# Kernel tuning notes

Measured on AMD Instinct MI355X. Metric: run time of the kernel, lower is better.

Reference implementation:

```python
import jax, jax.numpy as jnp
import numpy as np
import math

COV_WEIGHT = 1.0
BANDWIDTH_FACTOR = 1.06
SQRT_2PI = math.sqrt(2.0 * math.pi)
EPS_LOG = 1e-8
H_MIN = 1e-4


def setup_inputs() -> dict:
    key = jax.random.key(0)
    activity = jax.random.normal(key, (2048, 64), dtype=jnp.float32)
    return {"activity": activity}


def reference(activity):
    B, R = activity.shape
    # Silverman bandwidth per receptor (torch .std uses ddof=1)
    std = jnp.std(activity, axis=0, ddof=1)                     # (R,)
    h = jnp.maximum(BANDWIDTH_FACTOR * std * (B ** (-0.2)), H_MIN)  # (R,)

    # Pairwise Gaussian KDE: query == samples == activity
    u = (activity[:, None, :] - activity[None, :, :]) / h       # (B_q, B_s, R)
    kernel_values = jnp.exp(-0.5 * u * u) / SQRT_2PI             # (B_q, B_s, R)
    density = kernel_values.sum(axis=1) / (B * h)                # (B_q, R)

    entropies = -jnp.mean(jnp.log(density + EPS_LOG), axis=0)    # (R,)
    loss_entropy = -entropies.mean()

    # Covariance penalty: sum of squared off-diagonals
    centered = activity - activity.mean(axis=0, keepdims=True)
    cov = (centered.T @ centered) / (B - 1)                      # (R, R)
    off = cov - jnp.diag(jnp.diag(cov))
    loss_cov = jnp.sum(off * off)

    total_loss = loss_entropy + COV_WEIGHT * loss_cov
    return total_loss
```

## Files before the change

### kernel.cpp

```cpp
#include <hip/hip_runtime.h>
#include <math.h>

#define B_SZ 2048
#define R_SZ 64
#define QT 8
#define KDE_BLOCKS (B_SZ / QT)

#define B_POW_NEG02 0.217637640824031f
#define SQRT_2PI 2.5066282746310002f
#define LOG2E 1.44269504088896340736f

extern "C" __device__ float __ocml_native_exp2_f32(float);

typedef __attribute__((ext_vector_type(2))) float f32x2;


__global__ __launch_bounds__(1024) void stats_gram_kernel(const float* __restrict__ A,
                                                          float* __restrict__ qsums,
                                                          float* __restrict__ qsums2,
                                                          float* __restrict__ gram4,
                                                          float* __restrict__ ent_acc,
                                                          int* __restrict__ done_cnt) {
    int b = blockIdx.x;
    int i = b >> 2, qd = b & 3;
    int tid = threadIdx.x;
    int j = tid & 63, bg = tid >> 6;

    const float* __restrict__ Aq = A + (qd * 512) * R_SZ;
    float g = 0.f, sj = 0.f, s2j = 0.f;
#pragma unroll 4
    for (int t = bg; t < 512; t += 16) {
        float ai = Aq[t * R_SZ + i];
        float aj = Aq[t * R_SZ + j];
        g = fmaf(ai, aj, g);
        sj += aj;
        s2j = fmaf(aj, aj, s2j);
    }

    __shared__ float gred[16][64], sred[16][64], s2red[16][64];
    gred[bg][j] = g; sred[bg][j] = sj; s2red[bg][j] = s2j;
    __syncthreads();
    if (tid < 64) {
        float G = 0.f, S = 0.f, S2 = 0.f;
#pragma unroll
        for (int t = 0; t < 16; ++t) { G += gred[t][j]; S += sred[t][j]; S2 += s2red[t][j]; }
        gram4[b * 64 + j] = G;
        if (i == 0) {
            qsums[qd * 64 + j]  = S;
            qsums2[qd * 64 + j] = S2;
        }
    }
    if (b == 0 && tid == 64) { *ent_acc = 0.f; *done_cnt = 0; }
}

__global__ __launch_bounds__(1024) void kde_kernel(const float* __restrict__ A,
                                                   const float* __restrict__ qsums,
                                                   const float* __restrict__ qsums2,
                                                   const float* __restrict__ gram4,
                                                   float* __restrict__ ent_acc,
                                                   int* __restrict__ done_cnt,
                                                   float* __restrict__ out) {
    int tid = threadIdx.x;
    int r = tid & 63, sg = tid >> 6;

    __shared__ float k0s[64], lscs[64], sums_s[64];
    if (tid < 64) {
        float S  = qsums[tid]  + qsums[64 + tid]  + qsums[128 + tid]  + qsums[192 + tid];
        float S2 = qsums2[tid] + qsums2[64 + tid] + qsums2[128 + tid] + qsums2[192 + tid];
        float m = S * (1.f / (float)B_SZ);
        float var = (S2 - S * m) * (1.f / (float)(B_SZ - 1));
        var = fmaxf(var, 0.f);
        float h = fmaxf(1.06f * sqrtf(var) * B_POW_NEG02, 1e-4f);
        k0s[tid]  = sqrtf(0.5f * LOG2E) / h;
        lscs[tid] = 1.0f / ((float)B_SZ * h * SQRT_2PI);
        sums_s[tid] = S;
    }
    __syncthreads();
    float k0 = k0s[r];

    int q0 = blockIdx.x * QT;
    f32x2 uq01 = { A[(q0 + 0) * R_SZ + r] * k0, A[(q0 + 1) * R_SZ + r] * k0 };
    f32x2 uq23 = { A[(q0 + 2) * R_SZ + r] * k0, A[(q0 + 3) * R_SZ + r] * k0 };
    f32x2 uq45 = { A[(q0 + 4) * R_SZ + r] * k0, A[(q0 + 5) * R_SZ + r] * k0 };
    f32x2 uq67 = { A[(q0 + 6) * R_SZ + r] * k0, A[(q0 + 7) * R_SZ + r] * k0 };
    f32x2 c01 = { 0.f, 0.f }, c23 = { 0.f, 0.f };
    f32x2 c45 = { 0.f, 0.f }, c67 = { 0.f, 0.f };

#define KDE_BODY(usv)                                                          \
    {                                                                          \
        f32x2 uss = { (usv), (usv) };                                          \
        f32x2 d01 = uq01 - uss, d23 = uq23 - uss;                              \
        f32x2 d45 = uq45 - uss, d67 = uq67 - uss;                              \
        f32x2 n01 = -d01 * d01, n23 = -d23 * d23;                              \
        f32x2 n45 = -d45 * d45, n67 = -d67 * d67;                              \
        f32x2 e01 = { __ocml_native_exp2_f32(n01.x), __ocml_native_exp2_f32(n01.y) }; \
        f32x2 e23 = { __ocml_native_exp2_f32(n23.x), __ocml_native_exp2_f32(n23.y) }; \
        f32x2 e45 = { __ocml_native_exp2_f32(n45.x), __ocml_native_exp2_f32(n45.y) }; \
        f32x2 e67 = { __ocml_native_exp2_f32(n67.x), __ocml_native_exp2_f32(n67.y) }; \
        c01 += e01; c23 += e23; c45 += e45; c67 += e67;                        \
    }

    const float* __restrict__ Ap = A + sg * R_SZ + r;
    float p[8];
#pragma unroll
    for (int j = 0; j < 8; ++j) p[j] = Ap[j * 1024];

    int li = 8 * 1024;
#pragma unroll 1
    for (int k = 0; k < 15; ++k) {
#pragma unroll
        for (int j = 0; j < 8; ++j) {
            float us = p[j] * k0;
            p[j] = Ap[li + j * 1024];
            KDE_BODY(us);
        }
        li += 8 * 1024;
    }
#pragma unroll
    for (int j = 0; j < 8; ++j) { float us = p[j] * k0; KDE_BODY(us); }

#undef KDE_BODY

    __shared__ float red[16][QT][64];
    red[sg][0][r] = c01.x; red[sg][1][r] = c01.y;
    red[sg][2][r] = c23.x; red[sg][3][r] = c23.y;
    red[sg][4][r] = c45.x; red[sg][5][r] = c45.y;
    red[sg][6][r] = c67.x; red[sg][7][r] = c67.y;
    __syncthreads();
    __shared__ float wred[QT];
    if (sg < QT) {
        float S = 0.f;
#pragma unroll
        for (int t = 0; t < 16; ++t) S += red[t][sg][r];
        float v = __logf(fmaf(S, lscs[r], 1e-8f));
        for (int off = 32; off > 0; off >>= 1) v += __shfl_down(v, off, 64);
        if (r == 0) wred[sg] = v;
    }
    __syncthreads();
    __shared__ int lastflag;
    if (tid == 0) {
        float p2 = 0.f;
#pragma unroll
        for (int t = 0; t < QT; ++t) p2 += wred[t];
        p2 *= (1.0f / ((float)B_SZ * (float)R_SZ));
        atomicAdd(ent_acc, p2);
        __threadfence();
        int prev = atomicAdd(done_cnt, 1);
        lastflag = (prev == KDE_BLOCKS - 1);
    }
    __syncthreads();
    if (lastflag) {
        __threadfence();
        float v = 0.f;
#pragma unroll
        for (int c = tid; c < 4096; c += 1024) {
            int ii = c >> 6, jj = c & 63;
            const float* gp = gram4 + ii * 256 + jj;
            float G = gp[0] + gp[64] + gp[128] + gp[192];
            float mi = sums_s[ii] * (1.f / (float)B_SZ);
            float mj = sums_s[jj] * (1.f / (float)B_SZ);
            float cov = (G - (float)B_SZ * mi * mj) * (1.f / (float)(B_SZ - 1));
            if (ii != jj) v = fmaf(cov, cov, v);
        }
        for (int off = 32; off > 0; off >>= 1) v += __shfl_down(v, off, 64);
        __shared__ float wsum[16];
        if (r == 0) wsum[sg] = v;
        __syncthreads();
        if (tid == 0) {
            float C = 0.f;
#pragma unroll
            for (int t = 0; t < 16; ++t) C += wsum[t];
            float ent = __hip_atomic_load(ent_acc, __ATOMIC_ACQUIRE,
                                          __HIP_MEMORY_SCOPE_AGENT);
            out[0] = ent + C;
        }
    }
}

extern "C" void kernel_launch(void* const* d_in, const int* in_sizes, int n_in,
                              void* d_out, int out_size, void* d_ws, size_t ws_size,
                              hipStream_t stream) {
    const float* A = (const float*)d_in[0];
    float* out = (float*)d_out;

    float* wsf = (float*)d_ws;
    float* qsums   = wsf;
    float* qsums2  = wsf + 256;
    float* ent_acc = wsf + 640;
    int*   done_cnt = (int*)(wsf + 672);
    float* gram4   = wsf + 1024;

    stats_gram_kernel<<<256, 1024, 0, stream>>>(A, qsums, qsums2, gram4,
                                                ent_acc, done_cnt);
    kde_kernel<<<KDE_BLOCKS, 1024, 0, stream>>>(A, qsums, qsums2, gram4,
                                                ent_acc, done_cnt, out);
}
```

Baseline: 95.84 us.

## Split KDE sample range across two blocks per query group with atomic density merge

Each query group of 8 rows is now handled by two blocks, each covering half of the 2048 samples. Partial densities are merged with atomicAdd into a global buffer, and a per-group counter picks the second finisher to take the log and feed the entropy accumulator. The launch goes from 256 to 512 blocks, which should fill the GPU's compute units better than one block per group. The cost is extra global atomics, one more zero-initialised workspace buffer, and a longer chain of completion handshakes.

```diff
diff --git a/kernel.cpp b/kernel.cpp
--- a/kernel.cpp
+++ b/kernel.cpp
@@ -4,7 +4,9 @@
 #define B_SZ 2048
 #define R_SZ 64
 #define QT 8
-#define KDE_BLOCKS (B_SZ / QT)
+#define NQG (B_SZ / QT)
+#define KDE_BLOCKS (NQG * 2)
+#define FINAL_CNT NQG
 
 #define B_POW_NEG02 0.217637640824031f
 #define SQRT_2PI 2.5066282746310002f
@@ -20,7 +22,9 @@
                                                           float* __restrict__ qsums2,
                                                           float* __restrict__ gram4,
                                                           float* __restrict__ ent_acc,
-                                                          int* __restrict__ done_cnt) {
+                                                          int* __restrict__ done_cnt,
+                                                          int* __restrict__ qcnt,
+                                                          float* __restrict__ dens) {
     int b = blockIdx.x;
     int i = b >> 2, qd = b & 3;
     int tid = threadIdx.x;
@@ -37,6 +41,8 @@
         s2j = fmaf(aj, aj, s2j);
     }
 
+    if (tid < 512) dens[b * 512 + tid] = 0.f;
+
     __shared__ float gred[16][64], sred[16][64], s2red[16][64];
     gred[bg][j] = g; sred[bg][j] = sj; s2red[bg][j] = s2j;
     __syncthreads();
@@ -50,16 +56,21 @@
             qsums2[qd * 64 + j] = S2;
         }
     }
-    if (b == 0 && tid == 64) { *ent_acc = 0.f; *done_cnt = 0; }
+    if (b == 0) {
+        if (tid == 64 + 256) { *ent_acc = 0.f; *done_cnt = 0; }
+        if (tid < 256) qcnt[tid] = 0;
+    }
 }
 
-__global__ __launch_bounds__(1024) void kde_kernel(const float* __restrict__ A,
-                                                   const float* __restrict__ qsums,
-                                                   const float* __restrict__ qsums2,
-                                                   const float* __restrict__ gram4,
-                                                   float* __restrict__ ent_acc,
-                                                   int* __restrict__ done_cnt,
-                                                   float* __restrict__ out) {
+__global__ __launch_bounds__(1024, 8) void kde_kernel(const float* __restrict__ A,
+                                                      const float* __restrict__ qsums,
+                                                      const float* __restrict__ qsums2,
+                                                      const float* __restrict__ gram4,
+                                                      float* __restrict__ ent_acc,
+                                                      int* __restrict__ done_cnt,
+                                                      int* __restrict__ qcnt,
+                                                      float* __restrict__ dens,
+                                                      float* __restrict__ out) {
     int tid = threadIdx.x;
     int r = tid & 63, sg = tid >> 6;
 
@@ -78,7 +89,8 @@
     __syncthreads();
     float k0 = k0s[r];
 
-    int q0 = blockIdx.x * QT;
+    int qg = blockIdx.x >> 1, half = blockIdx.x & 1;
+    int q0 = qg * QT;
     f32x2 uq01 = { A[(q0 + 0) * R_SZ + r] * k0, A[(q0 + 1) * R_SZ + r] * k0 };
     f32x2 uq23 = { A[(q0 + 2) * R_SZ + r] * k0, A[(q0 + 3) * R_SZ + r] * k0 };
     f32x2 uq45 = { A[(q0 + 4) * R_SZ + r] * k0, A[(q0 + 5) * R_SZ + r] * k0 };
@@ -100,14 +112,14 @@
         c01 += e01; c23 += e23; c45 += e45; c67 += e67;                        \
     }
 
-    const float* __restrict__ Ap = A + sg * R_SZ + r;
+    const float* __restrict__ Ap = A + (half * 1024 + sg) * R_SZ + r;
     float p[8];
 #pragma unroll
     for (int j = 0; j < 8; ++j) p[j] = Ap[j * 1024];
 
     int li = 8 * 1024;
 #pragma unroll 1
-    for (int k = 0; k < 15; ++k) {
+    for (int k = 0; k < 7; ++k) {
 #pragma unroll
         for (int j = 0; j < 8; ++j) {
             float us = p[j] * k0;
@@ -127,52 +139,68 @@
     red[sg][4][r] = c45.x; red[sg][5][r] = c45.y;
     red[sg][6][r] = c67.x; red[sg][7][r] = c67.y;
     __syncthreads();
-    __shared__ float wred[QT];
     if (sg < QT) {
         float S = 0.f;
 #pragma unroll
         for (int t = 0; t < 16; ++t) S += red[t][sg][r];
-        float v = __logf(fmaf(S, lscs[r], 1e-8f));
-        for (int off = 32; off > 0; off >>= 1) v += __shfl_down(v, off, 64);
-        if (r == 0) wred[sg] = v;
-    }
-    __syncthreads();
-    __shared__ int lastflag;
+        atomicAdd(&dens[(q0 + sg) * 64 + r], S);
+    }
+    __syncthreads();
+    __shared__ int amlast;
     if (tid == 0) {
-        float p2 = 0.f;
-#pragma unroll
-        for (int t = 0; t < QT; ++t) p2 += wred[t];
-        p2 *= (1.0f / ((float)B_SZ * (float)R_SZ));
-        atomicAdd(ent_acc, p2);
         __threadfence();
-        int prev = atomicAdd(done_cnt, 1);
-        lastflag = (prev == KDE_BLOCKS - 1);
-    }
-    __syncthreads();
-    if (lastflag) {
+        int prev = atomicAdd(&qcnt[qg], 1);
+        amlast = (prev == 1);
+    }
+    __syncthreads();
+    if (amlast) {
         __threadfence();
-        float v = 0.f;
-#pragma unroll
-        for (int c = tid; c < 4096; c += 1024) {
-            int ii = c >> 6, jj = c & 63;
-            const float* gp = gram4 + ii * 256 + jj;
-            float G = gp[0] + gp[64] + gp[128] + gp[192];
-            float mi = sums_s[ii] * (1.f / (float)B_SZ);
-            float mj = sums_s[jj] * (1.f / (float)B_SZ);
-            float cov = (G - (float)B_SZ * mi * mj) * (1.f / (float)(B_SZ - 1));
-            if (ii != jj) v = fmaf(cov, cov, v);
-        }
-        for (int off = 32; off > 0; off >>= 1) v += __shfl_down(v, off, 64);
-        __shared__ float wsum[16];
-        if (r == 0) wsum[sg] = v;
+        __shared__ float wred[QT];
+        if (sg < QT) {
+            float Sf = __hip_atomic_load(&dens[(q0 + sg) * 64 + r],
+                                         __ATOMIC_RELAXED, __HIP_MEMORY_SCOPE_AGENT);
+            float v = __logf(fmaf(Sf, lscs[r], 1e-8f));
+            for (int off = 32; off > 0; off >>= 1) v += __shfl_down(v, off, 64);
+            if (r == 0) wred[sg] = v;
+        }
         __syncthreads();
+        __shared__ int lastflag;
         if (tid == 0) {
-            float C = 0.f;
-#pragma unroll
-            for (int t = 0; t < 16; ++t) C += wsum[t];
-            float ent = __hip_atomic_load(ent_acc, __ATOMIC_ACQUIRE,
-                                          __HIP_MEMORY_SCOPE_AGENT);
-            out[0] = ent + C;
+            float p2 = 0.f;
+#pragma unroll
+            for (int t = 0; t < QT; ++t) p2 += wred[t];
+            p2 *= (1.0f / ((float)B_SZ * (float)R_SZ));
+            atomicAdd(ent_acc, p2);
+            __threadfence();
+            int prev = atomicAdd(done_cnt, 1);
+            lastflag = (prev == FINAL_CNT - 1);
+        }
+        __syncthreads();
+        if (lastflag) {
+            __threadfence();
+            float v = 0.f;
+#pragma unroll
+            for (int c = tid; c < 4096; c += 1024) {
+                int ii = c >> 6, jj = c & 63;
+                const float* gp = gram4 + ii * 256 + jj;
+                float G = gp[0] + gp[64] + gp[128] + gp[192];
+                float mi = sums_s[ii] * (1.f / (float)B_SZ);
+                float mj = sums_s[jj] * (1.f / (float)B_SZ);
+                float cov = (G - (float)B_SZ * mi * mj) * (1.f / (float)(B_SZ - 1));
+                if (ii != jj) v = fmaf(cov, cov, v);
+            }
+            for (int off = 32; off > 0; off >>= 1) v += __shfl_down(v, off, 64);
+            __shared__ float wsum[16];
+            if (r == 0) wsum[sg] = v;
+            __syncthreads();
+            if (tid == 0) {
+                float C = 0.f;
+#pragma unroll
+                for (int t = 0; t < 16; ++t) C += wsum[t];
+                float ent = __hip_atomic_load(ent_acc, __ATOMIC_ACQUIRE,
+                                              __HIP_MEMORY_SCOPE_AGENT);
+                out[0] = ent + C;
+            }
         }
     }
 }
@@ -188,10 +216,12 @@
     float* qsums2  = wsf + 256;
     float* ent_acc = wsf + 640;
     int*   done_cnt = (int*)(wsf + 672);
+    int*   qcnt    = (int*)(wsf + 768);
     float* gram4   = wsf + 1024;
+    float* dens    = wsf + 20480;
 
     stats_gram_kernel<<<256, 1024, 0, stream>>>(A, qsums, qsums2, gram4,
-                                                ent_acc, done_cnt);
+                                                ent_acc, done_cnt, qcnt, dens);
     kde_kernel<<<KDE_BLOCKS, 1024, 0, stream>>>(A, qsums, qsums2, gram4,
-                                                ent_acc, done_cnt, out);
+                                                ent_acc, done_cnt, qcnt, dens, out);
 }
```

After: 188.9 us. 97.1% more time.
